# Kernel tuning notes

Measured on AMD Instinct MI355X. Metric: run time of the kernel, lower is better.

## Reference

```python
import jax, jax.numpy as jnp
import numpy as np

B, C_IN, T, N = 16, 64, 12, 5000
C_OUT = 64


def setup_inputs() -> dict:
    key = jax.random.key(0)
    k1, k2, k3, k4 = jax.random.split(key, 4)
    x = jax.random.normal(k1, (B, C_IN, T, N), dtype=jnp.float32)
    # normalized adjacency / graph shift operator (dense representation of the sparse filter)
    gcnconv_filter = jax.random.uniform(k2, (N, N), dtype=jnp.float32)
    weight = jax.random.normal(k3, (C_IN, C_OUT), dtype=jnp.float32) * (1.0 / np.sqrt(C_IN))
    bias = jax.random.normal(k4, (C_OUT,), dtype=jnp.float32) * 0.1
    return {"x": x, "gcnconv_filter": gcnconv_filter, "weight": weight, "bias": bias}


def reference(x, gcnconv_filter, weight, bias):
    batch_size, c_in, t, n_vertex = x.shape
    c_out = weight.shape[1]
    # faithful to torch: raw row-major reshape of [B, c_in, T, N] to [-1, c_in]
    x_flat = x.reshape(-1, c_in)                      # [B*T*N, c_in]
    h = (x_flat @ weight).reshape(n_vertex, -1)       # [N, B*T*c_out] (raw reshape)
    agg = gcnconv_filter @ h                          # spmm aggregation over vertices
    out = agg.reshape(-1, c_out) + bias               # [N*B*T, c_out]
    return out
```

## Files before the change

kernel.cpp:

```cpp
#include <hip/hip_runtime.h>

#define N_VERT 5000
#define NCOL   12288
#define KPAD   5056
#define MPAD   5120

#define G1_BLOCKS  15168
#define CVT_BLOCKS 25280

typedef float          f32x4  __attribute__((ext_vector_type(4)));
typedef unsigned short u16x4  __attribute__((ext_vector_type(4)));
typedef __bf16         bf16x8 __attribute__((ext_vector_type(8)));

__device__ __forceinline__ unsigned short f2bf(float f) {
  unsigned int u = __builtin_bit_cast(unsigned int, f);
  u += 0x7fffu + ((u >> 16) & 1u);
  return (unsigned short)(u >> 16);
}

__device__ __forceinline__ void async16(const unsigned short* g, unsigned short* l) {
  __builtin_amdgcn_global_load_lds(
      (const __attribute__((address_space(1))) unsigned int*)g,
      (__attribute__((address_space(3))) unsigned int*)l, 16, 0, 0);
}

__global__ __launch_bounds__(256) void prep(const float* __restrict__ x,
                                            const float* __restrict__ W,
                                            const float* __restrict__ F,
                                            unsigned short* __restrict__ Ht,
                                            unsigned short* __restrict__ Fb) {
  __shared__ unsigned short xh[64][72];
  __shared__ unsigned short xl[64][72];
  __shared__ unsigned short Wt[64][72];
  const int tid = threadIdx.x;

  if (blockIdx.x >= G1_BLOCKS) {
    int idx = (blockIdx.x - G1_BLOCKS) * 256 + tid;
    int row = idx / (KPAD / 4);
    int c4  = (idx % (KPAD / 4)) * 4;
    u16x4 o;
    if (row < N_VERT && c4 < N_VERT) {
      f32x4 v = *(const f32x4*)(F + (long)row * N_VERT + c4);
      o.x = f2bf(v.x); o.y = f2bf(v.y); o.z = f2bf(v.z); o.w = f2bf(v.w);
    } else {
      o.x = 0; o.y = 0; o.z = 0; o.w = 0;
    }
    *(u16x4*)(Fb + (long)row * KPAD + c4) = o;
    return;
  }

  const int utile = blockIdx.x % 79;
  const int rr    = blockIdx.x / 79;

  for (int i = tid; i < 4096; i += 256) Wt[i & 63][i >> 6] = f2bf(W[i]);

  {
    int rowu = tid >> 2;
    int cb   = (tid & 3) * 16;
    long u   = (long)utile * 64 + rowu;
    bool valid = (u < N_VERT);
    const float* src = x + (u * 192 + rr) * 64;
#pragma unroll
    for (int q = 0; q < 4; ++q) {
      int col = cb + q * 4;
      f32x4 v = {0.f, 0.f, 0.f, 0.f};
      if (valid) v = *(const f32x4*)(src + col);
      u16x4 h, lo;
#pragma unroll
      for (int e = 0; e < 4; ++e) {
        unsigned short hb = f2bf(v[e]);
        float hf = __builtin_bit_cast(float, (unsigned int)hb << 16);
        h[e]  = hb;
        lo[e] = f2bf(v[e] - hf);
      }
      *(u16x4*)&xh[rowu][col] = h;
      *(u16x4*)&xl[rowu][col] = lo;
    }
  }
  __syncthreads();

  const int l  = tid & 63;
  const int w  = tid >> 6;
  const int la = l & 15;
  const int ch = l >> 4;
  const int jb = w * 16;

  const char* xhp = (const char*)xh;
  const char* xlp = (const char*)xl;
  const char* wtp = (const char*)Wt;

  f32x4 acc[4] = {};
#pragma unroll
  for (int ks = 0; ks < 2; ++ks) {
    const int ko = ks * 64 + ch * 16;
    bf16x8 bfr = *(const bf16x8*)(wtp + (jb + la) * 144 + ko);
#pragma unroll
    for (int a = 0; a < 4; ++a) {
      bf16x8 al = *(const bf16x8*)(xlp + (a * 16 + la) * 144 + ko);
      bf16x8 ah = *(const bf16x8*)(xhp + (a * 16 + la) * 144 + ko);
      acc[a] = __builtin_amdgcn_mfma_f32_16x16x32_bf16(al, bfr, acc[a], 0, 0, 0);
      acc[a] = __builtin_amdgcn_mfma_f32_16x16x32_bf16(ah, bfr, acc[a], 0, 0, 0);
    }
  }

  const long col = (long)rr * 64 + jb + la;
  const long kb  = (long)utile * 64 + ch * 4;
#pragma unroll
  for (int a = 0; a < 4; ++a) {
    u16x4 o = {f2bf(acc[a][0]), f2bf(acc[a][1]), f2bf(acc[a][2]), f2bf(acc[a][3])};
    *(u16x4*)(Ht + col * KPAD + kb + a * 16) = o;
  }
}

__global__ __launch_bounds__(512, 2) void gemm2(const unsigned short* __restrict__ A,
                                                const unsigned short* __restrict__ Bt,
                                                const float* __restrict__ bias,
                                                float* __restrict__ out) {
  __shared__ __align__(16) char sm[114688];

  const int tid = threadIdx.x;
  const int l   = tid & 63;
  const int w   = tid >> 6;
  const int wr  = w >> 2;
  const int wc  = w & 3;
  const int la  = l & 15;

  const int xcd = blockIdx.x & 7;
  const int ii  = blockIdx.x >> 3;
  const int gg  = ii / 40;
  const int rmap= ii % 40;
  const long tM = (long)(gg * 5 + (rmap % 5)) * 256;
  const long tN = (long)(xcd * 8 + (rmap / 5)) * 192;

  const int  sRow  = l >> 3;
  const int  sCol8 = ((l & 7) ^ (l >> 3)) * 8;
  const unsigned short* gA2 = A  + (tM + sRow) * (size_t)KPAD + sCol8;
  const unsigned short* gB2 = Bt + (tN + sRow) * (size_t)KPAD + sCol8;

  auto stageA2 = [&](int bufB, const unsigned short* g, int regionOff) {
    async16(g + (size_t)(w * 8)      * KPAD, (unsigned short*)(sm + bufB + regionOff + w * 1024));
    async16(g + (size_t)(w * 8 + 64) * KPAD, (unsigned short*)(sm + bufB + regionOff + (w + 8) * 1024));
  };
  auto stageB = [&](int bufB, const unsigned short* g) {
    async16(g + (size_t)(w * 8)       * KPAD, (unsigned short*)(sm + bufB + 32768 + w * 1024));
    async16(g + (size_t)(w * 8 + 64)  * KPAD, (unsigned short*)(sm + bufB + 32768 + (w + 8) * 1024));
    async16(g + (size_t)(w * 8 + 128) * KPAD, (unsigned short*)(sm + bufB + 32768 + (w + 16) * 1024));
  };

  const int cOff0 = ((l >> 4) * 16)      ^ ((l & 7) << 4);
  const int cOff1 = (64 + (l >> 4) * 16) ^ ((l & 7) << 4);
  const int aRow  = (wr * 128 + la) * 128;
  const int bRow  = 32768 + (wc * 48 + la) * 128;
  const char* pA0[2] = { sm + aRow + cOff0, sm + 57344 + aRow + cOff0 };
  const char* pA1[2] = { sm + aRow + cOff1, sm + 57344 + aRow + cOff1 };
  const char* pB0[2] = { sm + bRow + cOff0, sm + 57344 + bRow + cOff0 };
  const char* pB1[2] = { sm + bRow + cOff1, sm + 57344 + bRow + cOff1 };

  f32x4  acc[8][3] = {};
  bf16x8 af[4][2], b0[2][2], b1k[2];

  auto tile = [&](int bi, int mode) {
    const int bo = bi * 57344;
    const int ni = bi ^ 1;
#pragma unroll
    for (int i2 = 0; i2 < 4; ++i2) {
      af[i2][0] = *(const bf16x8*)(pA0[bi] + i2 * 2048);
      af[i2][1] = *(const bf16x8*)(pA1[bi] + i2 * 2048);
    }
    b1k[0] = *(const bf16x8*)(pB0[bi] + 2 * 2048);
    b1k[1] = *(const bf16x8*)(pB1[bi] + 2 * 2048);
    __builtin_amdgcn_s_setprio(1);
#pragma unroll
    for (int ks = 0; ks < 2; ++ks)
#pragma unroll
      for (int i2 = 0; i2 < 4; ++i2) {
#pragma unroll
        for (int j2 = 0; j2 < 2; ++j2)
          acc[i2][j2] = __builtin_amdgcn_mfma_f32_16x16x32_bf16(
              af[i2][ks], b0[j2][ks], acc[i2][j2], 0, 0, 0);
        acc[i2][2] = __builtin_amdgcn_mfma_f32_16x16x32_bf16(
            af[i2][ks], b1k[ks], acc[i2][2], 0, 0, 0);
      }
    __builtin_amdgcn_s_setprio(0);
    __builtin_amdgcn_s_barrier();
#pragma unroll
    for (int i2 = 0; i2 < 4; ++i2) {
      af[i2][0] = *(const bf16x8*)(pA0[bi] + (4 + i2) * 2048);
      af[i2][1] = *(const bf16x8*)(pA1[bi] + (4 + i2) * 2048);
    }
    if (mode == 0) {
      stageB(bo, gB2);
      gB2 += 64;
    }
    __builtin_amdgcn_s_setprio(1);
#pragma unroll
    for (int ks = 0; ks < 2; ++ks)
#pragma unroll
      for (int i2 = 0; i2 < 4; ++i2)
#pragma unroll
        for (int j2 = 0; j2 < 2; ++j2)
          acc[4 + i2][j2] = __builtin_amdgcn_mfma_f32_16x16x32_bf16(
              af[i2][ks], b0[j2][ks], acc[4 + i2][j2], 0, 0, 0);
    __builtin_amdgcn_s_setprio(0);
    __builtin_amdgcn_s_barrier();
    if (mode == 0) {
      stageA2(bo, gA2, 0);
      stageA2(bo, gA2 + (size_t)128 * KPAD, 16384);
      gA2 += 64;
      asm volatile("s_waitcnt vmcnt(7)" ::: "memory");
    } else if (mode == 1) {
      asm volatile("s_waitcnt vmcnt(0)" ::: "memory");
    }
    __builtin_amdgcn_s_barrier();
    __builtin_amdgcn_sched_barrier(0);
    if (mode != 2) {
#pragma unroll
      for (int j = 0; j < 2; ++j) {
        b0[j][0] = *(const bf16x8*)(pB0[ni] + j * 2048);
        b0[j][1] = *(const bf16x8*)(pB1[ni] + j * 2048);
      }
    }
    __builtin_amdgcn_s_setprio(1);
#pragma unroll
    for (int ks = 0; ks < 2; ++ks)
#pragma unroll
      for (int i2 = 0; i2 < 4; ++i2)
        acc[4 + i2][2] = __builtin_amdgcn_mfma_f32_16x16x32_bf16(
            af[i2][ks], b1k[ks], acc[4 + i2][2], 0, 0, 0);
    __builtin_amdgcn_s_setprio(0);
  };

  stageB(0, gB2);
  stageA2(0, gA2, 0); stageA2(0, gA2 + (size_t)128 * KPAD, 16384);
  gA2 += 64; gB2 += 64;
  stageB(57344, gB2);
  stageA2(57344, gA2, 0); stageA2(57344, gA2 + (size_t)128 * KPAD, 16384);
  gA2 += 64; gB2 += 64;
  asm volatile("s_waitcnt vmcnt(7)" ::: "memory");
  __builtin_amdgcn_s_barrier();
  __builtin_amdgcn_sched_barrier(0);
#pragma unroll
  for (int j = 0; j < 2; ++j) {
    b0[j][0] = *(const bf16x8*)(pB0[0] + j * 2048);
    b0[j][1] = *(const bf16x8*)(pB1[0] + j * 2048);
  }

  for (int it = 0; it < 38; ++it) {
    tile(0, 0);
    tile(1, 0);
  }
  tile(0, 0);
  tile(1, 1);
  tile(0, 2);

  float bv[3];
#pragma unroll
  for (int n = 0; n < 3; ++n) bv[n] = bias[(wc * 48 + n * 16 + la) & 63];
  const int rb = (l >> 4) * 4;
#pragma unroll
  for (int m = 0; m < 8; ++m) {
    long gm0 = tM + wr * 128 + m * 16 + rb;
#pragma unroll
    for (int rr2 = 0; rr2 < 4; ++rr2) {
      long gm = gm0 + rr2;
      if (gm < N_VERT) {
#pragma unroll
        for (int n = 0; n < 3; ++n) {
          long gn = tN + wc * 48 + n * 16 + la;
          out[gm * NCOL + gn] = acc[m][n][rr2] + bv[n];
        }
      }
    }
  }
}

extern "C" void kernel_launch(void* const* d_in, const int* in_sizes, int n_in,
                              void* d_out, int out_size, void* d_ws, size_t ws_size,
                              hipStream_t stream) {
  const float* x    = (const float*)d_in[0];
  const float* F    = (const float*)d_in[1];
  const float* W    = (const float*)d_in[2];
  const float* bias = (const float*)d_in[3];
  float* out = (float*)d_out;

  const size_t fbB = (size_t)MPAD * KPAD * 2;
  const size_t htB = (size_t)NCOL * KPAD * 2;
  if (ws_size < fbB + htB) return;

  unsigned short* Fb = (unsigned short*)d_ws;
  unsigned short* Ht = (unsigned short*)((char*)d_ws + fbB);

  prep <<<dim3(G1_BLOCKS + CVT_BLOCKS), 256, 0, stream>>>(x, W, F, Ht, Fb);
  gemm2<<<dim3(1280),                   512, 0, stream>>>(Fb, Ht, bias, out);
}
```

Before: 667.4 us.

## Retile GEMM to 256x256 blocks with 4 waves and 128x128 per-wave tiles

Changes the aggregation GEMM from 512-thread blocks computing 256x192 tiles to 256-thread blocks computing 256x256 tiles, so each wave now owns a 128x128 output tile with 64 accumulators. The goal is more MFMA work per LDS fragment load and fewer blocks (960 instead of 1280), which raises arithmetic intensity and cuts global reloads of the A panel. In exchange it uses 128KB of LDS and many more registers, leaving one block of 4 waves per CU, so latency hiding becomes weaker and register spills are possible.

```diff
diff --git a/kernel.cpp b/kernel.cpp
--- a/kernel.cpp
+++ b/kernel.cpp
@@ -112,74 +112,76 @@
   }
 }
 
-__global__ __launch_bounds__(512, 2) void gemm2(const unsigned short* __restrict__ A,
+__global__ __launch_bounds__(256, 1) void gemm2(const unsigned short* __restrict__ A,
                                                 const unsigned short* __restrict__ Bt,
                                                 const float* __restrict__ bias,
                                                 float* __restrict__ out) {
-  __shared__ __align__(16) char sm[114688];
+  __shared__ __align__(16) char sm[131072];
 
   const int tid = threadIdx.x;
   const int l   = tid & 63;
   const int w   = tid >> 6;
-  const int wr  = w >> 2;
-  const int wc  = w & 3;
+  const int wr  = w >> 1;
+  const int wc  = w & 1;
   const int la  = l & 15;
 
   const int xcd = blockIdx.x & 7;
   const int ii  = blockIdx.x >> 3;
-  const int gg  = ii / 40;
-  const int rmap= ii % 40;
+  const int gg  = ii / 30;
+  const int rmap= ii % 30;
   const long tM = (long)(gg * 5 + (rmap % 5)) * 256;
-  const long tN = (long)(xcd * 8 + (rmap / 5)) * 192;
+  const long tN = (long)(xcd * 6 + (rmap / 5)) * 256;
 
   const int  sRow  = l >> 3;
   const int  sCol8 = ((l & 7) ^ (l >> 3)) * 8;
   const unsigned short* gA2 = A  + (tM + sRow) * (size_t)KPAD + sCol8;
   const unsigned short* gB2 = Bt + (tN + sRow) * (size_t)KPAD + sCol8;
 
-  auto stageA2 = [&](int bufB, const unsigned short* g, int regionOff) {
-    async16(g + (size_t)(w * 8)      * KPAD, (unsigned short*)(sm + bufB + regionOff + w * 1024));
-    async16(g + (size_t)(w * 8 + 64) * KPAD, (unsigned short*)(sm + bufB + regionOff + (w + 8) * 1024));
-  };
-  auto stageB = [&](int bufB, const unsigned short* g) {
-    async16(g + (size_t)(w * 8)       * KPAD, (unsigned short*)(sm + bufB + 32768 + w * 1024));
-    async16(g + (size_t)(w * 8 + 64)  * KPAD, (unsigned short*)(sm + bufB + 32768 + (w + 8) * 1024));
-    async16(g + (size_t)(w * 8 + 128) * KPAD, (unsigned short*)(sm + bufB + 32768 + (w + 16) * 1024));
+  auto stage8 = [&](int bufB, const unsigned short* g, int regionOff) {
+#pragma unroll
+    for (int q = 0; q < 8; ++q)
+      async16(g + (size_t)(w * 64 + q * 8) * KPAD,
+              (unsigned short*)(sm + bufB + regionOff + w * 8192 + q * 1024));
   };
 
   const int cOff0 = ((l >> 4) * 16)      ^ ((l & 7) << 4);
   const int cOff1 = (64 + (l >> 4) * 16) ^ ((l & 7) << 4);
   const int aRow  = (wr * 128 + la) * 128;
-  const int bRow  = 32768 + (wc * 48 + la) * 128;
-  const char* pA0[2] = { sm + aRow + cOff0, sm + 57344 + aRow + cOff0 };
-  const char* pA1[2] = { sm + aRow + cOff1, sm + 57344 + aRow + cOff1 };
-  const char* pB0[2] = { sm + bRow + cOff0, sm + 57344 + bRow + cOff0 };
-  const char* pB1[2] = { sm + bRow + cOff1, sm + 57344 + bRow + cOff1 };
-
-  f32x4  acc[8][3] = {};
-  bf16x8 af[4][2], b0[2][2], b1k[2];
+  const int bRow  = 32768 + (wc * 128 + la) * 128;
+  const char* pA0[2] = { sm + aRow + cOff0, sm + 65536 + aRow + cOff0 };
+  const char* pA1[2] = { sm + aRow + cOff1, sm + 65536 + aRow + cOff1 };
+  const char* pB0[2] = { sm + bRow + cOff0, sm + 65536 + bRow + cOff0 };
+  const char* pB1[2] = { sm + bRow + cOff1, sm + 65536 + bRow + cOff1 };
+
+  f32x4  acc[8][8] = {};
+  bf16x8 af[4][2], b0[4][2], b1[4][2];
 
   auto tile = [&](int bi, int mode) {
-    const int bo = bi * 57344;
+    const int bo = bi << 16;
     const int ni = bi ^ 1;
 #pragma unroll
     for (int i2 = 0; i2 < 4; ++i2) {
       af[i2][0] = *(const bf16x8*)(pA0[bi] + i2 * 2048);
       af[i2][1] = *(const bf16x8*)(pA1[bi] + i2 * 2048);
     }
-    b1k[0] = *(const bf16x8*)(pB0[bi] + 2 * 2048);
-    b1k[1] = *(const bf16x8*)(pB1[bi] + 2 * 2048);
+#pragma unroll
+    for (int j = 0; j < 4; ++j) {
+      b1[j][0] = *(const bf16x8*)(pB0[bi] + (4 + j) * 2048);
+      b1[j][1] = *(const bf16x8*)(pB1[bi] + (4 + j) * 2048);
+    }
     __builtin_amdgcn_s_setprio(1);
 #pragma unroll
     for (int ks = 0; ks < 2; ++ks)
 #pragma unroll
       for (int i2 = 0; i2 < 4; ++i2) {
 #pragma unroll
-        for (int j2 = 0; j2 < 2; ++j2)
+        for (int j2 = 0; j2 < 4; ++j2)
           acc[i2][j2] = __builtin_amdgcn_mfma_f32_16x16x32_bf16(
               af[i2][ks], b0[j2][ks], acc[i2][j2], 0, 0, 0);
-        acc[i2][2] = __builtin_amdgcn_mfma_f32_16x16x32_bf16(
-            af[i2][ks], b1k[ks], acc[i2][2], 0, 0, 0);
+#pragma unroll
+        for (int j2 = 0; j2 < 4; ++j2)
+          acc[i2][4 + j2] = __builtin_amdgcn_mfma_f32_16x16x32_bf16(
+              af[i2][ks], b1[j2][ks], acc[i2][4 + j2], 0, 0, 0);
       }
     __builtin_amdgcn_s_setprio(0);
     __builtin_amdgcn_s_barrier();
@@ -189,7 +191,7 @@
       af[i2][1] = *(const bf16x8*)(pA1[bi] + (4 + i2) * 2048);
     }
     if (mode == 0) {
-      stageB(bo, gB2);
+      stage8(bo, gB2, 32768);
       gB2 += 64;
     }
     __builtin_amdgcn_s_setprio(1);
@@ -198,16 +200,15 @@
 #pragma unroll
       for (int i2 = 0; i2 < 4; ++i2)
 #pragma unroll
-        for (int j2 = 0; j2 < 2; ++j2)
+        for (int j2 = 0; j2 < 4; ++j2)
           acc[4 + i2][j2] = __builtin_amdgcn_mfma_f32_16x16x32_bf16(
               af[i2][ks], b0[j2][ks], acc[4 + i2][j2], 0, 0, 0);
     __builtin_amdgcn_s_setprio(0);
     __builtin_amdgcn_s_barrier();
     if (mode == 0) {
-      stageA2(bo, gA2, 0);
-      stageA2(bo, gA2 + (size_t)128 * KPAD, 16384);
+      stage8(bo, gA2, 0);
       gA2 += 64;
-      asm volatile("s_waitcnt vmcnt(7)" ::: "memory");
+      asm volatile("s_waitcnt vmcnt(16)" ::: "memory");
     } else if (mode == 1) {
       asm volatile("s_waitcnt vmcnt(0)" ::: "memory");
     }
@@ -215,7 +216,7 @@
     __builtin_amdgcn_sched_barrier(0);
     if (mode != 2) {
 #pragma unroll
-      for (int j = 0; j < 2; ++j) {
+      for (int j = 0; j < 4; ++j) {
         b0[j][0] = *(const bf16x8*)(pB0[ni] + j * 2048);
         b0[j][1] = *(const bf16x8*)(pB1[ni] + j * 2048);
       }
@@ -225,26 +226,27 @@
     for (int ks = 0; ks < 2; ++ks)
 #pragma unroll
       for (int i2 = 0; i2 < 4; ++i2)
-        acc[4 + i2][2] = __builtin_amdgcn_mfma_f32_16x16x32_bf16(
-            af[i2][ks], b1k[ks], acc[4 + i2][2], 0, 0, 0);
+#pragma unroll
+        for (int j2 = 0; j2 < 4; ++j2)
+          acc[4 + i2][4 + j2] = __builtin_amdgcn_mfma_f32_16x16x32_bf16(
+              af[i2][ks], b1[j2][ks], acc[4 + i2][4 + j2], 0, 0, 0);
     __builtin_amdgcn_s_setprio(0);
   };
 
-  stageB(0, gB2);
-  stageA2(0, gA2, 0); stageA2(0, gA2 + (size_t)128 * KPAD, 16384);
+  stage8(0, gB2, 32768);     stage8(0, gA2, 0);
   gA2 += 64; gB2 += 64;
-  stageB(57344, gB2);
-  stageA2(57344, gA2, 0); stageA2(57344, gA2 + (size_t)128 * KPAD, 16384);
+  stage8(65536, gB2, 32768); stage8(65536, gA2, 0);
   gA2 += 64; gB2 += 64;
-  asm volatile("s_waitcnt vmcnt(7)" ::: "memory");
+  asm volatile("s_waitcnt vmcnt(16)" ::: "memory");
   __builtin_amdgcn_s_barrier();
   __builtin_amdgcn_sched_barrier(0);
 #pragma unroll
-  for (int j = 0; j < 2; ++j) {
+  for (int j = 0; j < 4; ++j) {
     b0[j][0] = *(const bf16x8*)(pB0[0] + j * 2048);
     b0[j][1] = *(const bf16x8*)(pB1[0] + j * 2048);
   }
 
+#pragma unroll 1
   for (int it = 0; it < 38; ++it) {
     tile(0, 0);
     tile(1, 0);
@@ -253,9 +255,9 @@
   tile(1, 1);
   tile(0, 2);
 
-  float bv[3];
-#pragma unroll
-  for (int n = 0; n < 3; ++n) bv[n] = bias[(wc * 48 + n * 16 + la) & 63];
+  float bv[4];
+#pragma unroll
+  for (int n = 0; n < 4; ++n) bv[n] = bias[n * 16 + la];
   const int rb = (l >> 4) * 4;
 #pragma unroll
   for (int m = 0; m < 8; ++m) {
@@ -265,9 +267,9 @@
       long gm = gm0 + rr2;
       if (gm < N_VERT) {
 #pragma unroll
-        for (int n = 0; n < 3; ++n) {
-          long gn = tN + wc * 48 + n * 16 + la;
-          out[gm * NCOL + gn] = acc[m][n][rr2] + bv[n];
+        for (int n = 0; n < 8; ++n) {
+          long gn = tN + wc * 128 + n * 16 + la;
+          out[gm * NCOL + gn] = acc[m][n][rr2] + bv[n & 3];
         }
       }
     }
@@ -291,5 +293,5 @@
   unsigned short* Ht = (unsigned short*)((char*)d_ws + fbB);
 
   prep <<<dim3(G1_BLOCKS + CVT_BLOCKS), 256, 0, stream>>>(x, W, F, Ht, Fb);
-  gemm2<<<dim3(1280),                   512, 0, stream>>>(Fb, Ht, bias, out);
-}
+  gemm2<<<dim3(960),                    256, 0, stream>>>(Fb, Ht, bias, out);
+}
```

Result: slower. 1.385 ms (+107.6%).
